# Optimization experiments

Measured on AMD Instinct MI355X. Metric: run time of the kernel, lower is better.

Reference implementation:

```python
import jax, jax.numpy as jnp
import numpy as np

SEQ_LEN = 20   # fixed by the 18/19/20-position loop in get_each_word_feature
EMB = 768
FEAT = 512
EPS = 1e-12    # F.normalize eps


def _conv_relu(x, W, b):
    # x: [bs, L, 768]; W: [K, 768, C]; b: [C]
    # Equivalent to Conv2d(1, C, (K, 768)) on x.unsqueeze(1), then ReLU+squeeze.
    K = W.shape[0]
    L = x.shape[1]
    out = b
    for j in range(K):  # K in {1,2,3}: tiny static loop
        out = out + jnp.einsum('bld,dc->blc', x[:, j:L - K + 1 + j], W[j])
    return jax.nn.relu(out)  # [bs, L-K+1, C]


def _l2norm(x, axis):
    n = jnp.sqrt(jnp.sum(x * x, axis=axis, keepdims=True))
    return x / jnp.maximum(n, EPS)


def setup_inputs() -> dict:
    key = jax.random.key(0)
    ks = jax.random.split(key, 10)
    bs = 4096
    s = 0.02
    return {
        'words_emb': jax.random.normal(ks[0], (bs, SEQ_LEN, EMB), jnp.float32),
        'sent_emb': jax.random.normal(ks[1], (bs, EMB), jnp.float32),
        'W1': jax.random.normal(ks[2], (1, EMB, FEAT), jnp.float32) * s,
        'b1': jnp.zeros((FEAT,), jnp.float32),
        'W2': jax.random.normal(ks[3], (2, EMB, FEAT), jnp.float32) * s,
        'b2': jnp.zeros((FEAT,), jnp.float32),
        'W3': jax.random.normal(ks[4], (3, EMB, FEAT), jnp.float32) * s,
        'b3': jnp.zeros((FEAT,), jnp.float32),
        'Wp': jax.random.normal(ks[5], (EMB, FEAT), jnp.float32) * s,
        'bp': jnp.zeros((FEAT,), jnp.float32),
    }


def reference(words_emb, sent_emb, W1, b1, W2, b2, W3, b3, Wp, bp):
    # sentence projection (ProjectionHead.forward applies only the Linear)
    sent = sent_emb @ Wp + bp                       # [bs, C]

    # Bert_Word_Mapping: three 1D convs over tokens, kernel widths 1/2/3
    a = _conv_relu(words_emb, W1, b1)               # [bs, 20, C]
    b_ = _conv_relu(words_emb, W2, b2)              # [bs, 19, C]
    c = _conv_relu(words_emb, W3, b3)               # [bs, 18, C]

    # get_each_word_feature, vectorized: positional max over available convs.
    # ReLU outputs are >= 0, so zero-padding short sequences makes the
    # elementwise max reproduce the original per-position stack+amax exactly.
    b_pad = jnp.pad(b_, ((0, 0), (0, 1), (0, 0)))   # [bs, 20, C]
    c_pad = jnp.pad(c, ((0, 0), (0, 2), (0, 0)))    # [bs, 20, C]
    code = jnp.maximum(jnp.maximum(a, b_pad), c_pad)
    code = _l2norm(code, axis=2)                    # normalize over feature dim
    words_out = jnp.transpose(code, (0, 2, 1))      # [bs, C, 20]

    # get_word_feature: global max-pool over token dim, mean of 3, L2 norm
    pooled = (a.max(axis=1) + b_.max(axis=1) + c.max(axis=1)) / 3.0  # [bs, C]
    word_vector = _l2norm(pooled, axis=1)

    return (words_out, word_vector, sent)
```

## Files before the change

kernel.cpp:

```cpp
#include <hip/hip_runtime.h>
#include <hip/hip_bf16.h>
#include <stdint.h>

typedef __bf16 bf16_t;
typedef __bf16 bf16x8 __attribute__((ext_vector_type(8)));
typedef float f32x4 __attribute__((ext_vector_type(4)));

#define BS       4096
#define CB       1024
#define NCHUNK   4
#define SEQ      20
#define SEQP     22
#define EMB      768
#define FEAT     512
#define MC       (CB*SEQ)
#define KA       2304
#define WV_BASE   (41943040L)
#define SENT_BASE (44040192L)

#define BT_OFF    0L
#define WPT_OFF   7077888L
#define SENTX_OFF 7864320L
#define XPAD_OFF  14155776L
#define P_OFF     48758784L
#define WS_NEED   111673344L

__device__ __forceinline__ void async_copy16(void* lds, const void* g) {
  __builtin_amdgcn_global_load_lds(
      (__attribute__((address_space(1))) void*)(void*)g,
      (__attribute__((address_space(3))) void*)lds,
      16, 0, 0);
}

__global__ void pack_xpad(const float* __restrict__ words, bf16_t* __restrict__ Xpad) {
  long idx4 = ((long)blockIdx.x * blockDim.x + threadIdx.x) * 4;
  long row = idx4 / EMB;
  int  d   = (int)(idx4 % EMB);
  long b   = row / SEQP;
  int  r   = (int)(row % SEQP);
  ushort4 o;
  if (r < SEQ) {
    float4 v = *(const float4*)(words + ((b * SEQ + r) * EMB + d));
    o.x = __builtin_bit_cast(unsigned short, (bf16_t)v.x);
    o.y = __builtin_bit_cast(unsigned short, (bf16_t)v.y);
    o.z = __builtin_bit_cast(unsigned short, (bf16_t)v.z);
    o.w = __builtin_bit_cast(unsigned short, (bf16_t)v.w);
  } else {
    o.x = 0; o.y = 0; o.z = 0; o.w = 0;
  }
  *(ushort4*)(&Xpad[idx4]) = o;
}

__global__ void pack_sent(const float* __restrict__ sent, bf16_t* __restrict__ Xs) {
  long idx4 = ((long)blockIdx.x * blockDim.x + threadIdx.x) * 4;
  float4 v = *(const float4*)(sent + idx4);
  ushort4 o;
  o.x = __builtin_bit_cast(unsigned short, (bf16_t)v.x);
  o.y = __builtin_bit_cast(unsigned short, (bf16_t)v.y);
  o.z = __builtin_bit_cast(unsigned short, (bf16_t)v.z);
  o.w = __builtin_bit_cast(unsigned short, (bf16_t)v.w);
  *(ushort4*)(&Xs[idx4]) = o;
}

__global__ void pack_bt(const float* __restrict__ W1, const float* __restrict__ W2,
                        const float* __restrict__ W3, bf16_t* __restrict__ Bt) {
  long idx = (long)blockIdx.x * blockDim.x + threadIdx.x;
  int n = (int)(idx / KA), k = (int)(idx % KA);
  int g = n >> 9, c = n & 511;
  int j = k / EMB, d = k % EMB;
  float v = 0.f;
  if (j <= g) {
    const float* W = (g == 0) ? W1 : ((g == 1) ? W2 : W3);
    v = W[((long)j * EMB + d) * FEAT + c];
  }
  Bt[idx] = (bf16_t)v;
}

__global__ void pack_wpt(const float* __restrict__ Wp, bf16_t* __restrict__ Wpt) {
  long idx = (long)blockIdx.x * blockDim.x + threadIdx.x;
  int n = (int)(idx / EMB), k = (int)(idx % EMB);
  Wpt[idx] = (bf16_t)Wp[(long)k * FEAT + n];
}

template <int MODE>
__global__ __launch_bounds__(256, 2)
void gemm_k(const bf16_t* __restrict__ A, const bf16_t* __restrict__ Bt,
            const float* __restrict__ bias1, const float* __restrict__ bias2,
            const float* __restrict__ bias3,
            bf16_t* __restrict__ P, float* __restrict__ S) {
  constexpr int LDB = (MODE == 0) ? KA : EMB;
  __shared__ bf16_t As[128 * 64];
  __shared__ bf16_t Bs[128 * 64];

  const int tid  = threadIdx.x;
  const int lane = tid & 63;
  const int w    = tid >> 6;
  const int m0   = blockIdx.x * 128;
  const int n0t  = blockIdx.y * 128;

  int g, Keff;
  if (MODE == 0) { g = blockIdx.y >> 2; Keff = EMB * (g + 1); }
  else           { g = 0;               Keff = EMB; }

  long agbase[4], bgbase[4];
  int  ldsoff[4];
  #pragma unroll
  for (int i = 0; i < 4; i++) {
    int r = w * 32 + i * 8 + (lane >> 3);
    int cg = (lane & 7) ^ (r & 7);
    int m = m0 + r;
    long rowstart = (MODE == 0) ? ((long)(m / SEQ) * SEQP + (m % SEQ)) : (long)m;
    agbase[i] = rowstart * EMB + cg * 8;
    int n = n0t + r;
    bgbase[i] = (long)n * LDB + cg * 8;
    ldsoff[i] = (w * 32 + i * 8) * 64;
  }

  const int wm = w >> 1, wn = w & 1;
  const int q = lane >> 4, ln = lane & 15;
  int aoff[4][2], boff[4][2];
  #pragma unroll
  for (int t = 0; t < 4; t++) {
    int ra = wm * 64 + t * 16 + ln;
    int rb = wn * 64 + t * 16 + ln;
    #pragma unroll
    for (int ks = 0; ks < 2; ks++) {
      int c = ks * 4 + q;
      aoff[t][ks] = ra * 64 + ((c ^ (ra & 7)) * 8);
      boff[t][ks] = rb * 64 + ((c ^ (rb & 7)) * 8);
    }
  }

  f32x4 acc[4][4];
  #pragma unroll
  for (int i = 0; i < 4; i++)
    #pragma unroll
    for (int j = 0; j < 4; j++) acc[i][j] = (f32x4)0.f;

  for (int kb = 0; kb < Keff; kb += 64) {
    #pragma unroll
    for (int i = 0; i < 4; i++) {
      async_copy16(&As[ldsoff[i]], A  + agbase[i] + kb);
      async_copy16(&Bs[ldsoff[i]], Bt + bgbase[i] + kb);
    }
    __syncthreads();
    #pragma unroll
    for (int ks = 0; ks < 2; ks++) {
      bf16x8 af[4], bfr[4];
      #pragma unroll
      for (int t = 0; t < 4; t++) af[t]  = *(const bf16x8*)&As[aoff[t][ks]];
      #pragma unroll
      for (int t = 0; t < 4; t++) bfr[t] = *(const bf16x8*)&Bs[boff[t][ks]];
      #pragma unroll
      for (int mt = 0; mt < 4; mt++)
        #pragma unroll
        for (int nt = 0; nt < 4; nt++)
          acc[mt][nt] = __builtin_amdgcn_mfma_f32_16x16x32_bf16(af[mt], bfr[nt], acc[mt][nt], 0, 0, 0);
    }
    __syncthreads();
  }

  if (MODE == 0) {
    const float* bias = (g == 0) ? bias1 : ((g == 1) ? bias2 : bias3);
    int cbase = n0t - g * FEAT + wn * 64;
    #pragma unroll
    for (int nt = 0; nt < 4; nt++) {
      int c = cbase + nt * 16 + ln;
      float bv = bias[c];
      #pragma unroll
      for (int mt = 0; mt < 4; mt++) {
        int mrow = m0 + wm * 64 + mt * 16 + q * 4;
        #pragma unroll
        for (int v = 0; v < 4; v++) {
          int m = mrow + v;
          int l = m % SEQ;
          float val = acc[mt][nt][v] + bv;
          val = val > 0.f ? val : 0.f;
          if (l >= SEQ - g) val = 0.f;
          P[((long)g * MC + m) * FEAT + c] = (bf16_t)val;
        }
      }
    }
  } else {
    #pragma unroll
    for (int nt = 0; nt < 4; nt++) {
      int c = n0t + wn * 64 + nt * 16 + ln;
      float bv = bias1[c];
      #pragma unroll
      for (int mt = 0; mt < 4; mt++) {
        int mrow = m0 + wm * 64 + mt * 16 + q * 4;
        #pragma unroll
        for (int v = 0; v < 4; v++)
          S[(long)(mrow + v) * FEAT + c] = acc[mt][nt][v] + bv;
      }
    }
  }
}

__global__ __launch_bounds__(256)
void epilogue_k(const bf16_t* __restrict__ P, float* __restrict__ out, int b0) {
  const int bl = blockIdx.x;
  const long b = b0 + bl;
  const int t = threadIdx.x;
  const int lane = t & 63, w = t >> 6;
  const int c0 = t * 2;

  float code[SEQ][2];
  #pragma unroll
  for (int l = 0; l < SEQ; l++) { code[l][0] = 0.f; code[l][1] = 0.f; }
  float mg[3][2];

  #pragma unroll
  for (int gg = 0; gg < 3; gg++) {
    float mx0 = 0.f, mx1 = 0.f;
    #pragma unroll
    for (int l = 0; l < SEQ; l++) {
      uint32_t u = *(const uint32_t*)&P[((long)gg * MC + (long)bl * SEQ + l) * FEAT + c0];
      float v0 = __builtin_bit_cast(float, u << 16);
      float v1 = __builtin_bit_cast(float, u & 0xffff0000u);
      code[l][0] = fmaxf(code[l][0], v0);
      code[l][1] = fmaxf(code[l][1], v1);
      mx0 = fmaxf(mx0, v0); mx1 = fmaxf(mx1, v1);
    }
    mg[gg][0] = mx0; mg[gg][1] = mx1;
  }

  __shared__ float red[SEQ][4];
  __shared__ float redp[4];

  #pragma unroll
  for (int l = 0; l < SEQ; l++) {
    float s = code[l][0] * code[l][0] + code[l][1] * code[l][1];
    #pragma unroll
    for (int off = 32; off; off >>= 1) s += __shfl_xor(s, off, 64);
    if (lane == 0) red[l][w] = s;
  }
  float p0 = (mg[0][0] + mg[1][0] + mg[2][0]) * (1.f / 3.f);
  float p1 = (mg[0][1] + mg[1][1] + mg[2][1]) * (1.f / 3.f);
  float sp = p0 * p0 + p1 * p1;
  #pragma unroll
  for (int off = 32; off; off >>= 1) sp += __shfl_xor(sp, off, 64);
  if (lane == 0) redp[w] = sp;
  __syncthreads();

  float rnorm[SEQ];
  #pragma unroll
  for (int l = 0; l < SEQ; l++) {
    float s = red[l][0] + red[l][1] + red[l][2] + red[l][3];
    rnorm[l] = 1.f / fmaxf(sqrtf(s), 1e-12f);
  }
  float sP = redp[0] + redp[1] + redp[2] + redp[3];
  float rnp = 1.f / fmaxf(sqrtf(sP), 1e-12f);

  #pragma unroll
  for (int cc = 0; cc < 2; cc++) {
    long base = b * (FEAT * SEQ) + (long)(c0 + cc) * SEQ;
    #pragma unroll
    for (int l0 = 0; l0 < SEQ; l0 += 4) {
      float4 v;
      v.x = code[l0 + 0][cc] * rnorm[l0 + 0];
      v.y = code[l0 + 1][cc] * rnorm[l0 + 1];
      v.z = code[l0 + 2][cc] * rnorm[l0 + 2];
      v.w = code[l0 + 3][cc] * rnorm[l0 + 3];
      *(float4*)&out[base + l0] = v;
    }
  }
  out[WV_BASE + b * FEAT + c0]     = p0 * rnp;
  out[WV_BASE + b * FEAT + c0 + 1] = p1 * rnp;
}

extern "C" void kernel_launch(void* const* d_in, const int* in_sizes, int n_in,
                              void* d_out, int out_size, void* d_ws, size_t ws_size,
                              hipStream_t stream) {
  const float* words = (const float*)d_in[0];
  const float* sent  = (const float*)d_in[1];
  const float* W1 = (const float*)d_in[2];
  const float* b1 = (const float*)d_in[3];
  const float* W2 = (const float*)d_in[4];
  const float* b2 = (const float*)d_in[5];
  const float* W3 = (const float*)d_in[6];
  const float* b3 = (const float*)d_in[7];
  const float* Wp = (const float*)d_in[8];
  const float* bp = (const float*)d_in[9];
  float* out = (float*)d_out;
  char* ws = (char*)d_ws;

  if (ws_size < (size_t)WS_NEED) return;

  bf16_t* Bt    = (bf16_t*)(ws + BT_OFF);
  bf16_t* Wpt   = (bf16_t*)(ws + WPT_OFF);
  bf16_t* sentX = (bf16_t*)(ws + SENTX_OFF);
  bf16_t* Xpad  = (bf16_t*)(ws + XPAD_OFF);
  bf16_t* P     = (bf16_t*)(ws + P_OFF);

  pack_bt<<<13824, 256, 0, stream>>>(W1, W2, W3, Bt);
  pack_wpt<<<1536, 256, 0, stream>>>(Wp, Wpt);
  pack_sent<<<3072, 256, 0, stream>>>(sent, sentX);
  gemm_k<1><<<dim3(32, 4), 256, 0, stream>>>(sentX, Wpt, bp, bp, bp, nullptr, out + SENT_BASE);

  for (int ch = 0; ch < NCHUNK; ch++) {
    int b0 = ch * CB;
    pack_xpad<<<16896, 256, 0, stream>>>(words + (long)b0 * SEQ * EMB, Xpad);
    gemm_k<0><<<dim3(160, 12), 256, 0, stream>>>(Xpad, Bt, b1, b2, b3, P, nullptr);
    epilogue_k<<<CB, 256, 0, stream>>>(P, out, b0);
  }
}
```

Measured before the change: 972.4 us.

## Replace conv GEMM with 256x256 8-wave pipelined kernel and single-chunk path

Replaces the 128x128 conv GEMM with a 512-thread 256x256-tile kernel. It double-buffers LDS with async global-to-LDS loads, splits each K step into four phased MFMA blocks with barriers and raised priority, and remaps workgroup IDs for cache locality. When the workspace is large enough, all 4096 batches are processed in one chunk instead of four, which cuts launch count and tail effects. The costs are 128KB of LDS per block and a larger workspace requirement on the full path.

```diff
diff --git a/kernel.cpp b/kernel.cpp
--- a/kernel.cpp
+++ b/kernel.cpp
@@ -7,13 +7,10 @@
 typedef float f32x4 __attribute__((ext_vector_type(4)));
 
 #define BS       4096
-#define CB       1024
-#define NCHUNK   4
 #define SEQ      20
 #define SEQP     22
 #define EMB      768
 #define FEAT     512
-#define MC       (CB*SEQ)
 #define KA       2304
 #define WV_BASE   (41943040L)
 #define SENT_BASE (44040192L)
@@ -22,8 +19,8 @@
 #define WPT_OFF   7077888L
 #define SENTX_OFF 7864320L
 #define XPAD_OFF  14155776L
-#define P_OFF     48758784L
-#define WS_NEED   111673344L
+#define WS_MIN    111673344L
+#define WS_FULL   404226048L
 
 __device__ __forceinline__ void async_copy16(void* lds, const void* g) {
   __builtin_amdgcn_global_load_lds(
@@ -82,13 +79,9 @@
   Wpt[idx] = (bf16_t)Wp[(long)k * FEAT + n];
 }
 
-template <int MODE>
 __global__ __launch_bounds__(256, 2)
-void gemm_k(const bf16_t* __restrict__ A, const bf16_t* __restrict__ Bt,
-            const float* __restrict__ bias1, const float* __restrict__ bias2,
-            const float* __restrict__ bias3,
-            bf16_t* __restrict__ P, float* __restrict__ S) {
-  constexpr int LDB = (MODE == 0) ? KA : EMB;
+void gemm_sent(const bf16_t* __restrict__ A, const bf16_t* __restrict__ Bt,
+               const float* __restrict__ bias, float* __restrict__ S) {
   __shared__ bf16_t As[128 * 64];
   __shared__ bf16_t Bs[128 * 64];
 
@@ -98,21 +91,14 @@
   const int m0   = blockIdx.x * 128;
   const int n0t  = blockIdx.y * 128;
 
-  int g, Keff;
-  if (MODE == 0) { g = blockIdx.y >> 2; Keff = EMB * (g + 1); }
-  else           { g = 0;               Keff = EMB; }
-
   long agbase[4], bgbase[4];
   int  ldsoff[4];
   #pragma unroll
   for (int i = 0; i < 4; i++) {
     int r = w * 32 + i * 8 + (lane >> 3);
     int cg = (lane & 7) ^ (r & 7);
-    int m = m0 + r;
-    long rowstart = (MODE == 0) ? ((long)(m / SEQ) * SEQP + (m % SEQ)) : (long)m;
-    agbase[i] = rowstart * EMB + cg * 8;
-    int n = n0t + r;
-    bgbase[i] = (long)n * LDB + cg * 8;
+    agbase[i] = (long)(m0 + r) * EMB + cg * 8;
+    bgbase[i] = (long)(n0t + r) * EMB + cg * 8;
     ldsoff[i] = (w * 32 + i * 8) * 64;
   }
 
@@ -137,7 +123,7 @@
     #pragma unroll
     for (int j = 0; j < 4; j++) acc[i][j] = (f32x4)0.f;
 
-  for (int kb = 0; kb < Keff; kb += 64) {
+  for (int kb = 0; kb < EMB; kb += 64) {
     #pragma unroll
     for (int i = 0; i < 4; i++) {
       async_copy16(&As[ldsoff[i]], A  + agbase[i] + kb);
@@ -160,45 +146,198 @@
     __syncthreads();
   }
 
-  if (MODE == 0) {
-    const float* bias = (g == 0) ? bias1 : ((g == 1) ? bias2 : bias3);
-    int cbase = n0t - g * FEAT + wn * 64;
-    #pragma unroll
-    for (int nt = 0; nt < 4; nt++) {
-      int c = cbase + nt * 16 + ln;
-      float bv = bias[c];
+  #pragma unroll
+  for (int nt = 0; nt < 4; nt++) {
+    int c = n0t + wn * 64 + nt * 16 + ln;
+    float bv = bias[c];
+    #pragma unroll
+    for (int mt = 0; mt < 4; mt++) {
+      int mrow = m0 + wm * 64 + mt * 16 + q * 4;
       #pragma unroll
-      for (int mt = 0; mt < 4; mt++) {
-        int mrow = m0 + wm * 64 + mt * 16 + q * 4;
-        #pragma unroll
-        for (int v = 0; v < 4; v++) {
-          int m = mrow + v;
-          int l = m % SEQ;
-          float val = acc[mt][nt][v] + bv;
-          val = val > 0.f ? val : 0.f;
-          if (l >= SEQ - g) val = 0.f;
-          P[((long)g * MC + m) * FEAT + c] = (bf16_t)val;
-        }
+      for (int v = 0; v < 4; v++)
+        S[(long)(mrow + v) * FEAT + c] = acc[mt][nt][v] + bv;
+    }
+  }
+}
+
+
+#define MM4(MH, I, AV)                                                                               \
+  acc[(MH)*4+(I)][0] = __builtin_amdgcn_mfma_f32_16x16x32_bf16(AV, b0_, acc[(MH)*4+(I)][0], 0, 0, 0); \
+  acc[(MH)*4+(I)][1] = __builtin_amdgcn_mfma_f32_16x16x32_bf16(AV, b1_, acc[(MH)*4+(I)][1], 0, 0, 0); \
+  acc[(MH)*4+(I)][2] = __builtin_amdgcn_mfma_f32_16x16x32_bf16(AV, b2_, acc[(MH)*4+(I)][2], 0, 0, 0); \
+  acc[(MH)*4+(I)][3] = __builtin_amdgcn_mfma_f32_16x16x32_bf16(AV, b3_, acc[(MH)*4+(I)][3], 0, 0, 0);
+
+#define ARD(MH, AB)                                                  \
+    bf16x8 a0_ = *(const bf16x8*)&smem[(AB) + aoff[MH][0]];          \
+    bf16x8 a1_ = *(const bf16x8*)&smem[(AB) + aoff[MH][1]];          \
+    bf16x8 a2_ = *(const bf16x8*)&smem[(AB) + aoff[MH][2]];          \
+    bf16x8 a3_ = *(const bf16x8*)&smem[(AB) + aoff[MH][3]];
+
+#define BRD(BB)                                                      \
+    b0_ = *(const bf16x8*)&smem[(BB) + boff[0]];                     \
+    b1_ = *(const bf16x8*)&smem[(BB) + boff[1]];                     \
+    b2_ = *(const bf16x8*)&smem[(BB) + boff[2]];                     \
+    b3_ = *(const bf16x8*)&smem[(BB) + boff[3]];
+
+#define PH_SYNC()                                                    \
+    __builtin_amdgcn_s_barrier();                                    \
+    asm volatile("s_waitcnt lgkmcnt(0)" ::: "memory");               \
+    __builtin_amdgcn_sched_barrier(0);                               \
+    __builtin_amdgcn_s_setprio(1)
+
+#define PH_END()                                                     \
+    __builtin_amdgcn_s_setprio(0);                                   \
+    __builtin_amdgcn_s_barrier()
+
+__global__ __launch_bounds__(512, 2)
+void gemm8(const bf16_t* __restrict__ Axp, const bf16_t* __restrict__ Bt,
+           const float* __restrict__ bias1, const float* __restrict__ bias2,
+           const float* __restrict__ bias3, bf16_t* __restrict__ P, int Mtot) {
+  __shared__ bf16_t smem[65536];
+
+  const int tid  = threadIdx.x;
+  const int lane = tid & 63, w = tid >> 6;
+  const int wm = w >> 2, wn = w & 3;
+  const int ln = lane & 15, q = lane >> 4;
+  const int wbase = w * 512;
+
+  const int nx   = gridDim.x;
+  const int nwg  = nx * 6;
+  const int orig = blockIdx.y * nx + blockIdx.x;
+  const int wgid = (orig & 7) * (nwg >> 3) + (orig >> 3);
+  const int bx = wgid / 6, by = wgid % 6;
+  const int m0  = bx * 256;
+  const int n0t = by * 256;
+  const int g   = by >> 1;
+  const int NT  = 12 * (g + 1);
+
+  long aSrc0, aSrc1, bSrc0, bSrc1;
+  {
+    int pair = (tid >> 3);
+    int u    = (tid & 7) ^ (pair & 7);
+    int row  = pair * 2 + (u >> 2);
+    int c    = u & 3;
+    int m    = m0 + row;
+    aSrc0 = ((long)(m / SEQ) * SEQP + (m % SEQ)) * EMB + c * 8;
+    bSrc0 = (long)(n0t + row) * KA + c * 8;
+    pair += 64;
+    u   = (tid & 7) ^ (pair & 7);
+    row = pair * 2 + (u >> 2);
+    c   = u & 3;
+    m   = m0 + row;
+    aSrc1 = ((long)(m / SEQ) * SEQP + (m % SEQ)) * EMB + c * 8;
+    bSrc1 = (long)(n0t + row) * KA + c * 8;
+  }
+
+  auto stA = [&](int buf, int ks, int kb) {
+    const int rb = buf * 32768 + ks * 8192;
+    async_copy16(&smem[rb + wbase],        Axp + aSrc0 + kb + ks * 32);
+    async_copy16(&smem[rb + 4096 + wbase], Axp + aSrc1 + kb + ks * 32);
+  };
+  auto stB = [&](int buf, int ks, int kb) {
+    const int rb = buf * 32768 + 16384 + ks * 8192;
+    async_copy16(&smem[rb + wbase],        Bt + bSrc0 + kb + ks * 32);
+    async_copy16(&smem[rb + 4096 + wbase], Bt + bSrc1 + kb + ks * 32);
+  };
+
+  int aoff[2][4], boff[4];
+  #pragma unroll
+  for (int mh = 0; mh < 2; mh++)
+    #pragma unroll
+    for (int t4 = 0; t4 < 4; t4++) {
+      int r = wm * 128 + mh * 64 + t4 * 16 + ln;
+      int slot = (q | ((r & 1) << 2)) ^ ((r >> 1) & 7);
+      aoff[mh][t4] = (r >> 1) * 64 + slot * 8;
+    }
+  #pragma unroll
+  for (int nf = 0; nf < 4; nf++) {
+    int r = wn * 64 + nf * 16 + ln;
+    int slot = (q | ((r & 1) << 2)) ^ ((r >> 1) & 7);
+    boff[nf] = (r >> 1) * 64 + slot * 8;
+  }
+
+  f32x4 acc[8][4];
+  #pragma unroll
+  for (int i = 0; i < 8; i++)
+    #pragma unroll
+    for (int j = 0; j < 4; j++) acc[i][j] = (f32x4)0.f;
+
+  stA(0, 0, 0);
+  stA(0, 1, 0);
+  stB(0, 0, 0);
+  stB(0, 1, 0);
+  stB(1, 0, 64);
+  stA(1, 0, 64);
+  stB(1, 1, 64);
+  asm volatile("s_waitcnt vmcnt(6)" ::: "memory");
+  __builtin_amdgcn_s_barrier();
+
+  for (int t = 0; t < NT; ++t) {
+    const int cb  = (t & 1) << 15;
+    const int ab0 = cb, ab1 = cb + 8192;
+    const int bb0 = cb + 16384, bb1 = cb + 24576;
+    const int nb  = (t & 1) ^ 1;
+    bf16x8 b0_, b1_, b2_, b3_;
+
+    {
+      ARD(0, ab0)
+      BRD(bb0)
+      if (t + 1 < NT) stA(nb, 1, (t + 1) * 64);
+      PH_SYNC();
+      MM4(0, 0, a0_) MM4(0, 1, a1_) MM4(0, 2, a2_) MM4(0, 3, a3_)
+      PH_END();
+    }
+    {
+      ARD(1, ab0)
+      if (t + 2 < NT) stB(t & 1, 0, (t + 2) * 64);
+      PH_SYNC();
+      MM4(1, 0, a0_) MM4(1, 1, a1_) MM4(1, 2, a2_) MM4(1, 3, a3_)
+      PH_END();
+    }
+    {
+      ARD(0, ab1)
+      BRD(bb1)
+      if (t + 2 < NT) stA(t & 1, 0, (t + 2) * 64);
+      PH_SYNC();
+      MM4(0, 0, a0_) MM4(0, 1, a1_) MM4(0, 2, a2_) MM4(0, 3, a3_)
+      PH_END();
+    }
+    {
+      ARD(1, ab1)
+      if (t + 2 < NT) stB(t & 1, 1, (t + 2) * 64);
+      PH_SYNC();
+      MM4(1, 0, a0_) MM4(1, 1, a1_) MM4(1, 2, a2_) MM4(1, 3, a3_)
+      __builtin_amdgcn_s_setprio(0);
+      if (t + 2 < NT)      { asm volatile("s_waitcnt vmcnt(6)" ::: "memory"); }
+      else if (t + 1 < NT) { asm volatile("s_waitcnt vmcnt(0)" ::: "memory"); }
+      __builtin_amdgcn_s_barrier();
+    }
+  }
+
+  const float* bias = (g == 0) ? bias1 : ((g == 1) ? bias2 : bias3);
+  const int gc0 = (by & 1) * 256;
+  #pragma unroll
+  for (int nf = 0; nf < 4; nf++) {
+    int c = gc0 + wn * 64 + nf * 16 + ln;
+    float bv = bias[c];
+    #pragma unroll
+    for (int mf = 0; mf < 8; mf++) {
+      int mrow = m0 + wm * 128 + mf * 16 + q * 4;
+      #pragma unroll
+      for (int v = 0; v < 4; v++) {
+        int m = mrow + v;
+        int l = m % SEQ;
+        float val = acc[mf][nf][v] + bv;
+        val = val > 0.f ? val : 0.f;
+        if (l >= SEQ - g) val = 0.f;
+        P[((long)g * Mtot + m) * FEAT + c] = (bf16_t)val;
       }
     }
-  } else {
-    #pragma unroll
-    for (int nt = 0; nt < 4; nt++) {
-      int c = n0t + wn * 64 + nt * 16 + ln;
-      float bv = bias1[c];
-      #pragma unroll
-      for (int mt = 0; mt < 4; mt++) {
-        int mrow = m0 + wm * 64 + mt * 16 + q * 4;
-        #pragma unroll
-        for (int v = 0; v < 4; v++)
-          S[(long)(mrow + v) * FEAT + c] = acc[mt][nt][v] + bv;
-      }
-    }
   }
 }
 
 __global__ __launch_bounds__(256)
-void epilogue_k(const bf16_t* __restrict__ P, float* __restrict__ out, int b0) {
+void epilogue_k(const bf16_t* __restrict__ P, float* __restrict__ out, int b0, int Mtot) {
   const int bl = blockIdx.x;
   const long b = b0 + bl;
   const int t = threadIdx.x;
@@ -215,7 +354,7 @@
     float mx0 = 0.f, mx1 = 0.f;
     #pragma unroll
     for (int l = 0; l < SEQ; l++) {
-      uint32_t u = *(const uint32_t*)&P[((long)gg * MC + (long)bl * SEQ + l) * FEAT + c0];
+      uint32_t u = *(const uint32_t*)&P[((long)gg * Mtot + (long)bl * SEQ + l) * FEAT + c0];
       float v0 = __builtin_bit_cast(float, u << 16);
       float v1 = __builtin_bit_cast(float, u & 0xffff0000u);
       code[l][0] = fmaxf(code[l][0], v0);
@@ -285,23 +424,27 @@
   float* out = (float*)d_out;
   char* ws = (char*)d_ws;
 
-  if (ws_size < (size_t)WS_NEED) return;
-
+  int CBr, NCH;
+  if (ws_size >= (size_t)WS_FULL)     { CBr = 4096; NCH = 1; }
+  else if (ws_size >= (size_t)WS_MIN) { CBr = 1024; NCH = 4; }
+  else return;
+
+  const int Mtot = CBr * SEQ;
   bf16_t* Bt    = (bf16_t*)(ws + BT_OFF);
   bf16_t* Wpt   = (bf16_t*)(ws + WPT_OFF);
   bf16_t* sentX = (bf16_t*)(ws + SENTX_OFF);
   bf16_t* Xpad  = (bf16_t*)(ws + XPAD_OFF);
-  bf16_t* P     = (bf16_t*)(ws + P_OFF);
+  bf16_t* P     = (bf16_t*)(ws + XPAD_OFF + (long)CBr * SEQP * EMB * 2);
 
   pack_bt<<<13824, 256, 0, stream>>>(W1, W2, W3, Bt);
   pack_wpt<<<1536, 256, 0, stream>>>(Wp, Wpt);
   pack_sent<<<3072, 256, 0, stream>>>(sent, sentX);
-  gemm_k<1><<<dim3(32, 4), 256, 0, stream>>>(sentX, Wpt, bp, bp, bp, nullptr, out + SENT_BASE);
-
-  for (int ch = 0; ch < NCHUNK; ch++) {
-    int b0 = ch * CB;
-    pack_xpad<<<16896, 256, 0, stream>>>(words + (long)b0 * SEQ * EMB, Xpad);
-    gemm_k<0><<<dim3(160, 12), 256, 0, stream>>>(Xpad, Bt, b1, b2, b3, P, nullptr);
-    epilogue_k<<<CB, 256, 0, stream>>>(P, out, b0);
-  }
-}
+  gemm_sent<<<dim3(32, 4), 256, 0, stream>>>(sentX, Wpt, bp, out + SENT_BASE);
+
+  for (int ch = 0; ch < NCH; ch++) {
+    int b0 = ch * CBr;
+    pack_xpad<<<(CBr * SEQP * EMB) / 1024, 256, 0, stream>>>(words + (long)b0 * SEQ * EMB, Xpad);
+    gemm8<<<dim3(Mtot / 256, 6), 512, 0, stream>>>(Xpad, Bt, b1, b2, b3, P, Mtot);
+    epilogue_k<<<CBr, 256, 0, stream>>>(P, out, b0, Mtot);
+  }
+}
```

After: 933.0 us. -4.1%, faster.
